# Kernel tuning notes

Measured on AMD Instinct MI355X. Metric: run time of the kernel, lower is better.

## Reference

```python
import jax, jax.numpy as jnp
import numpy as np

LARGENUMBER = 10000.0
B, L = 32, 128


def setup_inputs() -> dict:
    key = jax.random.key(0)
    k1, k2 = jax.random.split(key)
    scores = jax.random.normal(k1, (B, L, L, 1), dtype=jnp.float32)
    seq_lens = jax.random.randint(k2, (B,), L // 2, L + 1).astype(jnp.int32)
    seq_lens = seq_lens.at[0].set(L)  # module assumes max(seq_lens) == matrix dim
    return {"span_mention_score_matrix": scores, "sequence_lengths": seq_lens}


def _inside_logZ(scores, seq_lens):
    """CKY inside algorithm in the log semiring (the `coolio` path).

    Recurrence (combined mention/non-mention channels):
      A[i,i]  = log(1 + e^{s_ii})
      A[i,j]  = logsumexp_{k=i..j-1}(A[i,k] + A[k+1,j]) + log(1 + e^{s_ij})
      Z[b]    = A[b, 0, len_b - 1]
    """
    s = scores[..., 0]                      # (B, L, L)
    Bn, Ln = s.shape[0], s.shape[1]
    log1p_exp = jnp.log1p(jnp.exp(s))       # log(1 + e^s), multiplicative factor per span
    # init: logsumexp([score, 0 above/on diag | -LARGE below diag]) as in coolio
    tri = jnp.where(jnp.arange(Ln)[:, None] <= jnp.arange(Ln)[None, :], 0.0, -LARGENUMBER)
    A0 = jnp.logaddexp(s, tri[None])        # diagonal entries = log(1+e^s); upper entries get overwritten

    i_idx = jnp.arange(Ln)[:, None]         # (L, 1)   span start
    m_idx = jnp.arange(Ln - 1)[None, :]     # (1, L-1) split offset
    rows = jnp.arange(Ln)

    def body(A, w):
        # left child  A[i, i+m], right child A[i+m+1, i+w], m = 0..w-1
        jl = jnp.clip(i_idx + m_idx, 0, Ln - 1)
        ir = jnp.clip(i_idx + m_idx + 1, 0, Ln - 1)
        jr = jnp.clip(i_idx + w, 0, Ln - 1)
        left = A[:, i_idx, jl]              # (B, L, L-1)
        right = A[:, ir, jr]                # (B, L, L-1)
        mask = (m_idx < w) & (i_idx + w < Ln)
        vals = jnp.where(mask, left + right, -LARGENUMBER)
        S = jax.nn.logsumexp(vals, axis=2)  # (B, L) logbmm along diagonal w
        cols = jnp.clip(rows + w, 0, N := Ln - 1) if False else jnp.clip(rows + w, 0, Ln - 1)
        new = S + log1p_exp[:, rows, cols]
        valid = (rows + w) < Ln
        A = A.at[:, rows, cols].set(jnp.where(valid[None, :], new, A[:, rows, cols]))
        return A, None

    A, _ = jax.lax.scan(body, A0, jnp.arange(1, Ln))
    Z = A[jnp.arange(Bn), 0, seq_lens - 1]  # (B,)
    return Z


def reference(span_mention_score_matrix, sequence_lengths):
    # forward returns (log-partition Z, marginals = dZ.sum()/dscores), like coolio()
    Z, vjp_fn = jax.vjp(lambda sc: _inside_logZ(sc, sequence_lengths), span_mention_score_matrix)
    marginal = vjp_fn(jnp.ones_like(Z))[0][..., 0]  # (B, L, L)
    return Z, marginal
```

## Files before the change

kernel.cpp:

```cpp
#include <hip/hip_runtime.h>

#define LL 128
#define STR 135
#define STR1 136
#define NT 1024

__device__ __forceinline__ float softplus_f(float x) { return log1pf(__expf(x)); }

extern "C" __global__ __launch_bounds__(NT, 1) void cky_kernel(
    const float* __restrict__ scores,
    const int* __restrict__ seq_lens,
    float* __restrict__ Z_out,
    float* __restrict__ marg_out)
{
    extern __shared__ float smem[];
    float* Al = smem;
    float* Gl = smem + LL * STR;
    float* DR = smem + 2 * LL * STR;

    const int b   = blockIdx.x;
    const int tid = threadIdx.x;
    const float* s = scores + (size_t)b * LL * LL;
    float* marg = marg_out + (size_t)b * LL * LL;
    const int len = seq_lens[b];

    for (int idx = tid; idx < LL * STR; idx += NT) Gl[idx] = 0.0f;
    if (tid < LL) DR[tid] = 0.0f;
    if (tid < len) Al[tid * STR + tid] = softplus_f(s[tid * LL + tid]);
    __syncthreads();

    for (int w = 1; w < len; ++w) {
        const int cells = len - w;
        const int clw = (w > 1) ? (32 - __clz(w - 1)) : 0;
        const int clc = (cells > 1) ? (32 - __clz(cells - 1)) : 0;
        int gsh = clw - 3; if (gsh < 0) gsh = 0;
        int cap = 10 - clc; if (gsh > cap) gsh = cap;
        if (gsh > 6) gsh = 6;
        const int g    = 1 << gsh;
        const int gid  = tid >> gsh;
        const int lane = tid & (g - 1);
        if (gid < cells) {
            const int i = gid, j = gid + w;
            const float sv = s[i * LL + j];
            const float M  = Al[i * STR + (j - 1)];
            const float* Arow = Al + i * STR1;
            const float* Acol = Al + (i + 1) * STR + j;
            float acc = 0.0f;
            const int m2 = 2 * lane;
            #pragma unroll
            for (int t = 0; t < 4; ++t) {
                if (2 * g * t < w) {
                    const int e = m2 + 2 * g * t;
                    float2 a2 = *(const float2*)(Arow + e);
                    float c0 = Acol[e * STR];
                    float c1 = Acol[(e + 1) * STR];
                    float e0 = __expf(a2.x + c0 - M);
                    float e1 = __expf(a2.y + c1 - M);
                    acc += (e     < w) ? e0 : 0.0f;
                    acc += (e + 1 < w) ? e1 : 0.0f;
                }
            }
            for (int off = g >> 1; off; off >>= 1)
                acc += __shfl_xor(acc, off, 64);
            if (lane == 0) {
                const float Sij = M + __logf(acc);
                Al[j * STR + i] = Sij;
                Al[i * STR + j] = Sij + softplus_f(sv);
            }
        }
        __syncthreads();
    }

    for (int w = len - 1; w >= 1; --w) {
        const int cells = len - w;
        const int clw = (w > 1) ? (32 - __clz(w - 1)) : 0;
        const int clc = (cells > 1) ? (32 - __clz(cells - 1)) : 0;
        int gsh = clw - 3; if (gsh < 0) gsh = 0;
        int cap = 10 - clc; if (gsh > cap) gsh = cap;
        if (gsh > 6) gsh = 6;
        const int g    = 1 << gsh;
        const int gid  = tid >> gsh;
        const int lane = tid & (g - 1);
        if (gid < cells) {
            const int i = gid, J = i + w;
            float Gp = Gl[i * STR + J] + Gl[J * STR + i];
            if (i == 0 && J == len - 1) Gp += 1.0f;
            if (Gp > 0.0f) {
                const float SL = Al[J * STR + i] - __logf(Gp);
                const float* Arow = Al + i * STR1;
                const float* Acol = Al + (i + 1) * STR + J;
                float*       Lrow = Gl + i * STR1;
                float*       Rrow = Gl + J * STR + i + 1;
                const int bulk = w - 1;
                const int m2 = 2 * lane;
                #pragma unroll
                for (int t = 0; t < 4; ++t) {
                    if ((t + 1) * 2 * g <= bulk) {
                        const int e = m2 + 2 * g * t;
                        float2 a2 = *(const float2*)(Arow + e);
                        float t0 = __expf(a2.x + Acol[e * STR]       - SL);
                        float t1 = __expf(a2.y + Acol[(e + 1) * STR] - SL);
                        float2 l2 = *(const float2*)(Lrow + e);
                        l2.x += t0; l2.y += t1;
                        *(float2*)(Lrow + e) = l2;
                        float r0 = Rrow[e] + t0;
                        float r1 = Rrow[e + 1] + t1;
                        Rrow[e] = r0; Rrow[e + 1] = r1;
                    }
                }
                const int e0 = (bulk / (2 * g)) * (2 * g);
                for (int e = e0 + lane; e < bulk; e += g) {
                    float tt = __expf(Arow[e] + Acol[e * STR] - SL);
                    Lrow[e] += tt;
                    Rrow[e] += tt;
                }
                if (lane == 0) {
                    float tt = __expf(Arow[w - 1] + Al[J * STR + J] - SL);
                    Lrow[w - 1] += tt;
                    DR[J]       += tt;
                }
            }
        }
        __syncthreads();
    }

    if (tid == 0) Z_out[b] = Al[0 * STR + (len - 1)];
    for (int idx = tid; idx < LL * LL; idx += NT) {
        const int r = idx >> 7, c = idx & (LL - 1);
        float G = 0.0f;
        if (c < len) {
            if (c > r)       G = Gl[r * STR + c] + Gl[c * STR + r];
            else if (c == r) G = Gl[r * STR + r] + DR[r];
            if (r == 0 && c == len - 1) G += 1.0f;
        }
        float m = 0.0f;
        if (G != 0.0f) {
            const float sv = s[idx];
            m = G / (1.0f + __expf(-sv));
        }
        marg[idx] = m;
    }
}

extern "C" void kernel_launch(void* const* d_in, const int* in_sizes, int n_in,
                              void* d_out, int out_size, void* d_ws, size_t ws_size,
                              hipStream_t stream) {
    const float* scores  = (const float*)d_in[0];
    const int* seq_lens  = (const int*)d_in[1];
    const int B = in_sizes[1];
    float* out = (float*)d_out;
    float* Z_out = out;
    float* marg  = out + B;

    const size_t lds_bytes = (size_t)(2 * LL * STR + LL) * sizeof(float);
    hipFuncSetAttribute((const void*)cky_kernel,
                        hipFuncAttributeMaxDynamicSharedMemorySize,
                        (int)lds_bytes);
    cky_kernel<<<B, NT, lds_bytes, stream>>>(scores, seq_lens, Z_out, marg);
}
```

Measured before the change: 323.5 us.

## Halve block size, cap group width at 16, use lightweight LDS barriers

Cuts the workgroup from 1024 to 512 threads and replaces the width-dependent group sizing with a cells-only rule capped at 16 lanes per cell. The fixed-trip unrolled inner loops become variable-trip loops with unroll 4 so long diagonals are still fully covered. __syncthreads is replaced with a custom LDS-only waitcnt plus s_barrier, which is meant to reduce per-step barrier cost across the roughly 250 sequential diagonal steps. The trade-off is fewer threads per step and more serial iterations per lane on wide diagonals, and the barrier now relies on the kernel's global reads not needing to be fenced.

```diff
diff --git a/kernel.cpp b/kernel.cpp
--- a/kernel.cpp
+++ b/kernel.cpp
@@ -3,9 +3,16 @@
 #define LL 128
 #define STR 135
 #define STR1 136
-#define NT 1024
+#define NT 512
+#define LARGENEG -1.0e30f
 
 __device__ __forceinline__ float softplus_f(float x) { return log1pf(__expf(x)); }
+
+__device__ __forceinline__ void lds_barrier() {
+    asm volatile("s_waitcnt lgkmcnt(0)" ::: "memory");
+    __builtin_amdgcn_s_barrier();
+    asm volatile("" ::: "memory");
+}
 
 extern "C" __global__ __launch_bounds__(NT, 1) void cky_kernel(
     const float* __restrict__ scores,
@@ -27,15 +34,12 @@
     for (int idx = tid; idx < LL * STR; idx += NT) Gl[idx] = 0.0f;
     if (tid < LL) DR[tid] = 0.0f;
     if (tid < len) Al[tid * STR + tid] = softplus_f(s[tid * LL + tid]);
-    __syncthreads();
+    lds_barrier();
 
     for (int w = 1; w < len; ++w) {
         const int cells = len - w;
-        const int clw = (w > 1) ? (32 - __clz(w - 1)) : 0;
         const int clc = (cells > 1) ? (32 - __clz(cells - 1)) : 0;
-        int gsh = clw - 3; if (gsh < 0) gsh = 0;
-        int cap = 10 - clc; if (gsh > cap) gsh = cap;
-        if (gsh > 6) gsh = 6;
+        int gsh = 9 - clc; if (gsh > 4) gsh = 4;
         const int g    = 1 << gsh;
         const int gid  = tid >> gsh;
         const int lane = tid & (g - 1);
@@ -47,18 +51,16 @@
             const float* Acol = Al + (i + 1) * STR + j;
             float acc = 0.0f;
             const int m2 = 2 * lane;
-            #pragma unroll
-            for (int t = 0; t < 4; ++t) {
-                if (2 * g * t < w) {
-                    const int e = m2 + 2 * g * t;
-                    float2 a2 = *(const float2*)(Arow + e);
-                    float c0 = Acol[e * STR];
-                    float c1 = Acol[(e + 1) * STR];
-                    float e0 = __expf(a2.x + c0 - M);
-                    float e1 = __expf(a2.y + c1 - M);
-                    acc += (e     < w) ? e0 : 0.0f;
-                    acc += (e + 1 < w) ? e1 : 0.0f;
-                }
+            #pragma unroll 4
+            for (int t = 0; 2 * g * t < w; ++t) {
+                const int e = m2 + 2 * g * t;
+                float2 a2 = *(const float2*)(Arow + e);
+                float c0 = Acol[e * STR];
+                float c1 = Acol[(e + 1) * STR];
+                float e0 = __expf(a2.x + c0 - M);
+                float e1 = __expf(a2.y + c1 - M);
+                acc += (e     < w) ? e0 : 0.0f;
+                acc += (e + 1 < w) ? e1 : 0.0f;
             }
             for (int off = g >> 1; off; off >>= 1)
                 acc += __shfl_xor(acc, off, 64);
@@ -68,16 +70,15 @@
                 Al[i * STR + j] = Sij + softplus_f(sv);
             }
         }
-        __syncthreads();
+        lds_barrier();
     }
+
+    if (tid == 0) Z_out[b] = Al[len - 1];
 
     for (int w = len - 1; w >= 1; --w) {
         const int cells = len - w;
-        const int clw = (w > 1) ? (32 - __clz(w - 1)) : 0;
         const int clc = (cells > 1) ? (32 - __clz(cells - 1)) : 0;
-        int gsh = clw - 3; if (gsh < 0) gsh = 0;
-        int cap = 10 - clc; if (gsh > cap) gsh = cap;
-        if (gsh > 6) gsh = 6;
+        int gsh = 9 - clc; if (gsh > 4) gsh = 4;
         const int g    = 1 << gsh;
         const int gid  = tid >> gsh;
         const int lane = tid & (g - 1);
@@ -93,20 +94,18 @@
                 float*       Rrow = Gl + J * STR + i + 1;
                 const int bulk = w - 1;
                 const int m2 = 2 * lane;
-                #pragma unroll
-                for (int t = 0; t < 4; ++t) {
-                    if ((t + 1) * 2 * g <= bulk) {
-                        const int e = m2 + 2 * g * t;
-                        float2 a2 = *(const float2*)(Arow + e);
-                        float t0 = __expf(a2.x + Acol[e * STR]       - SL);
-                        float t1 = __expf(a2.y + Acol[(e + 1) * STR] - SL);
-                        float2 l2 = *(const float2*)(Lrow + e);
-                        l2.x += t0; l2.y += t1;
-                        *(float2*)(Lrow + e) = l2;
-                        float r0 = Rrow[e] + t0;
-                        float r1 = Rrow[e + 1] + t1;
-                        Rrow[e] = r0; Rrow[e + 1] = r1;
-                    }
+                #pragma unroll 4
+                for (int t = 0; (t + 1) * 2 * g <= bulk; ++t) {
+                    const int e = m2 + 2 * g * t;
+                    float2 a2 = *(const float2*)(Arow + e);
+                    float t0 = __expf(a2.x + Acol[e * STR]       - SL);
+                    float t1 = __expf(a2.y + Acol[(e + 1) * STR] - SL);
+                    float2 l2 = *(const float2*)(Lrow + e);
+                    l2.x += t0; l2.y += t1;
+                    *(float2*)(Lrow + e) = l2;
+                    float r0 = Rrow[e] + t0;
+                    float r1 = Rrow[e + 1] + t1;
+                    Rrow[e] = r0; Rrow[e + 1] = r1;
                 }
                 const int e0 = (bulk / (2 * g)) * (2 * g);
                 for (int e = e0 + lane; e < bulk; e += g) {
@@ -121,10 +120,9 @@
                 }
             }
         }
-        __syncthreads();
+        lds_barrier();
     }
 
-    if (tid == 0) Z_out[b] = Al[0 * STR + (len - 1)];
     for (int idx = tid; idx < LL * LL; idx += NT) {
         const int r = idx >> 7, c = idx & (LL - 1);
         float G = 0.0f;
```

After: 320.5 us. Within noise of the previous version (-0.9%).
